# Performance work log

Measured on AMD Instinct MI355X. Metric: run time of the kernel, lower is better.

The kernel has to match this reference:

```python
import jax, jax.numpy as jnp
import numpy as np

B, D, NT, H, K = 4096, 112, 200, 512, 10
HID = 512
IN = 3 * D + NT + 1   # GRU input size = 537
M0 = H + 3 * D + NT   # MLP first-layer input = 1048


def setup_inputs() -> dict:
    key = jax.random.key(0)
    ks = jax.random.split(key, 9)
    def w(k, shape, fan):
        return jax.random.normal(k, shape, jnp.float32) / np.sqrt(fan).astype(np.float32)
    return {
        "z": jax.random.normal(ks[0], (B, D), jnp.float32),
        "c": jax.random.normal(ks[1], (B, D + NT), jnp.float32),
        "b": jax.random.uniform(ks[2], (B, D), jnp.float32),
        "m": jax.random.uniform(ks[3], (B, D), jnp.float32),
        "Wih": w(ks[4], (IN, 3 * H), IN),
        "Whh": w(ks[5], (H, 3 * H), H),
        "bih": jnp.zeros((3 * H,), jnp.float32),
        "bhh": jnp.zeros((3 * H,), jnp.float32),
        "W0": w(ks[6], (M0, HID), M0),
        "b0": jnp.zeros((HID,), jnp.float32),
        "W1": w(ks[7], (HID, HID), HID),
        "b1": jnp.zeros((HID,), jnp.float32),
        "W2": w(ks[8], (HID, 3 * K), HID),
        "b2": jnp.zeros((3 * K,), jnp.float32),
    }


def reference(z, c, b, m, Wih, Whh, bih, bhh, W0, b0, W1, b1, W2, b2):
    """AutoReg.logp: autoregressive GRU + MLP mixture-density head, gaussian base."""
    Bn = z.shape[0]
    const = jnp.concatenate([c, b, m], axis=1)          # [B, 3D+NT] fixed per step
    gi_const = const @ Wih[1:] + bih                    # input-proj of constant part
    w_z = Wih[0]                                        # [3H] weight for scalar z_t
    mlp_const = const @ W0[H:] + b0                     # const part of first MLP layer
    W0h = W0[:H]
    # teacher-forced previous-z sequence: z_0 = -1, then z[:, t-1]
    z_prev = jnp.concatenate([-jnp.ones((Bn, 1), z.dtype), z[:, :-1]], axis=1).T  # [D, B]

    def step(h, zt):  # h: [B,H], zt: [B]
        gi = zt[:, None] * w_z + gi_const               # [B, 3H]
        gh = h @ Whh + bhh
        ir, iz, inn = jnp.split(gi, 3, axis=1)
        hr, hz, hn = jnp.split(gh, 3, axis=1)
        r = jax.nn.sigmoid(ir + hr)
        u = jax.nn.sigmoid(iz + hz)
        n = jnp.tanh(inn + r * hn)
        h2 = (1.0 - u) * n + u * h                      # torch GRU update
        a = jnp.tanh(h2 @ W0h + mlp_const)              # Linear + Tanh on [h||c||b||m]
        a = jnp.tanh(a @ W1 + b1)
        p = a @ W2 + b2                                 # [B, 3K] mixture params
        return h2, p

    h0 = jnp.zeros((Bn, H), z.dtype)
    _, ps = jax.lax.scan(step, h0, z_prev)              # ps: [D, B, 3K]
    params = jnp.transpose(ps, (1, 0, 2))               # [B, D, 3K]

    logits, means, lsig = jnp.split(params, 3, axis=-1)
    sig = jnp.exp(lsig)
    t = z[..., None]
    log_norm = -lsig - 0.5 * np.float32(np.log(2.0 * np.pi))
    log_kern = -0.5 * jnp.square((t - means) / sig)
    ll = jax.nn.logsumexp(log_kern + log_norm + logits, axis=-1) \
         - jax.nn.logsumexp(logits, axis=-1)            # [B, D]

    query = m * (1.0 - b)
    mask = -jnp.sort(-query, axis=1)                    # descending sort values
    return jnp.sum(ll * mask, axis=1)                   # [B]
```

## Files before the change

kernel.cpp:

```cpp
#include <hip/hip_runtime.h>
#include <hip/hip_bf16.h>
#include <float.h>
#include <math.h>

#define BN   4096
#define DD   112
#define HH   512
#define G3   1536
#define CW   536
#define HIDD 512

typedef __attribute__((ext_vector_type(8))) short short8;
typedef __attribute__((ext_vector_type(4))) float float4v;

__device__ __forceinline__ unsigned short f2bf(float x) {
    __hip_bfloat16 h = __float2bfloat16(x);
    return *(unsigned short*)&h;
}

__global__ void build_const(const float* __restrict__ c, const float* __restrict__ b,
                            const float* __restrict__ m, float* __restrict__ out) {
    int idx = blockIdx.x * blockDim.x + threadIdx.x;
    if (idx >= BN * CW) return;
    int row = idx / CW, col = idx - row * CW;
    float v;
    if (col < 312)      v = c[row * 312 + col];
    else if (col < 424) v = b[row * 112 + (col - 312)];
    else                v = m[row * 112 + (col - 424)];
    out[idx] = v;
}

__global__ void zero_f32(float* __restrict__ p, int n) {
    int i = blockIdx.x * blockDim.x + threadIdx.x;
    if (i < n) p[i] = 0.0f;
}

__global__ __launch_bounds__(256) void gemm_bias(const float* __restrict__ A,
        const float* __restrict__ W, const float* __restrict__ bias,
        float* __restrict__ C, int N) {
    __shared__ float As[8][64];
    __shared__ float Ws[8][64];
    const int tid = threadIdx.x;
    const int tx = tid & 15, ty = tid >> 4;
    const int rowBase = blockIdx.x * 64, colBase = blockIdx.y * 64;
    float acc[4][4] = {};
    for (int kb = 0; kb < CW; kb += 8) {
        int l = tid * 2;
        {
            int i = l >> 3, j = l & 7;
            As[j][i] = A[(rowBase + i) * CW + kb + j];
            int i2 = (l + 1) >> 3, j2 = (l + 1) & 7;
            As[j2][i2] = A[(rowBase + i2) * CW + kb + j2];
        }
        {
            int j = l >> 6, n = l & 63;
            Ws[j][n] = W[(kb + j) * N + colBase + n];
            int j2 = (l + 1) >> 6, n2 = (l + 1) & 63;
            Ws[j2][n2] = W[(kb + j2) * N + colBase + n2];
        }
        __syncthreads();
#pragma unroll
        for (int k = 0; k < 8; ++k) {
            float av[4], wv[4];
#pragma unroll
            for (int i = 0; i < 4; ++i) av[i] = As[k][ty * 4 + i];
#pragma unroll
            for (int j = 0; j < 4; ++j) wv[j] = Ws[k][tx * 4 + j];
#pragma unroll
            for (int i = 0; i < 4; ++i)
#pragma unroll
                for (int j = 0; j < 4; ++j) acc[i][j] += av[i] * wv[j];
        }
        __syncthreads();
    }
#pragma unroll
    for (int i = 0; i < 4; ++i) {
        int r = rowBase + ty * 4 + i;
#pragma unroll
        for (int j = 0; j < 4; ++j) {
            int cc = colBase + tx * 4 + j;
            C[r * N + cc] = acc[i][j] + bias[cc];
        }
    }
}

__global__ void sort_mask(const float* __restrict__ b, const float* __restrict__ m,
                          float* __restrict__ maskbuf) {
    __shared__ float s[128];
    const int row = blockIdx.x, t = threadIdx.x;
    float v = -FLT_MAX;
    if (t < DD) v = m[row * DD + t] * (1.0f - b[row * DD + t]);
    s[t] = v;
    __syncthreads();
    for (int k = 2; k <= 128; k <<= 1) {
        for (int j = k >> 1; j > 0; j >>= 1) {
            int ixj = t ^ j;
            if (ixj > t) {
                bool up = ((t & k) == 0);
                float a = s[t], bb = s[ixj];
                if ((a > bb) == up) { s[t] = bb; s[ixj] = a; }
            }
            __syncthreads();
        }
    }
    if (t < DD) maskbuf[row * DD + t] = s[127 - t];
}

__global__ void pack_w(const float* __restrict__ src, unsigned short* __restrict__ dst,
                       int kchunks, int ldn, int ncols) {
    int bid = blockIdx.x;
    int nt = bid / kchunks, kc = bid - nt * kchunks;
    int lane = threadIdx.x;
    int quad = lane >> 4, l16 = lane & 15;
    int n = nt * 16 + l16;
    unsigned short v[8];
#pragma unroll
    for (int j = 0; j < 8; ++j) {
        int k = kc * 32 + quad * 8 + j;
        float f = (n < ncols) ? src[(size_t)k * ldn + n] : 0.0f;
        v[j] = f2bf(f);
    }
    unsigned short* p = dst + ((size_t)bid * 64 + lane) * 8;
#pragma unroll
    for (int j = 0; j < 8; ++j) p[j] = v[j];
}

__global__ __launch_bounds__(1024, 4) void gru_rec_chunk(
    const float* __restrict__ z, const float* __restrict__ Wih,
    const float* __restrict__ bhh, const float* __restrict__ gi_const,
    const unsigned short* __restrict__ WhhP,
    float* __restrict__ hstate, unsigned short* __restrict__ h2g,
    int t0, int tlen)
{
    __shared__ unsigned short h_bf[16 * 520];
    __shared__ float zbuf[113 * 16];

    const int tid = threadIdx.x;
    const int wave = tid >> 6, lane = tid & 63;
    const int quad = lane >> 4, l16 = lane & 15;
    const int rowBase = blockIdx.x * 16;

    for (int idx = tid; idx < 113 * 16; idx += 1024) {
        int tt = idx >> 4, r = idx & 15;
        zbuf[idx] = (tt == 0) ? -1.0f : z[(rowBase + r) * DD + tt - 1];
    }

    int hcol[2];
    float wz0[2], wz1[2], wz2[2], bh2r[2];
    float gic0[2][4], gic1[2][4], gic2[2][4];
    float h_own[2][4];
#pragma unroll
    for (int i = 0; i < 2; ++i) {
        int tile = wave + 16 * i;
        int hc = tile * 16 + l16;
        hcol[i] = hc;
        wz0[i] = Wih[hc]; wz1[i] = Wih[512 + hc]; wz2[i] = Wih[1024 + hc];
        float bh0 = bhh[hc], bh1 = bhh[512 + hc];
        bh2r[i] = bhh[1024 + hc];
#pragma unroll
        for (int rg = 0; rg < 4; ++rg) {
            int m = quad * 4 + rg;
            const float* g = gi_const + (size_t)(rowBase + m) * G3;
            gic0[i][rg] = g[hc] + bh0;
            gic1[i][rg] = g[512 + hc] + bh1;
            gic2[i][rg] = g[1024 + hc];
            float hv = hstate[(size_t)(rowBase + m) * HH + hc];
            h_own[i][rg] = hv;
            h_bf[m * 520 + hc] = f2bf(hv);
        }
    }
    const short8* WhhF = (const short8*)WhhP;
    __syncthreads();

    for (int tt = 0; tt < tlen; ++tt) {
        const int t = t0 + tt;
        float4v accR[2], accU[2], accN[2];
#pragma unroll
        for (int i = 0; i < 2; ++i) {
            accR[i] = (float4v){gic0[i][0], gic0[i][1], gic0[i][2], gic0[i][3]};
            accU[i] = (float4v){gic1[i][0], gic1[i][1], gic1[i][2], gic1[i][3]};
            accN[i] = (float4v){0.f, 0.f, 0.f, 0.f};
        }
#pragma unroll 4
        for (int kc = 0; kc < 16; ++kc) {
            short8 af = *(const short8*)&h_bf[l16 * 520 + kc * 32 + quad * 8];
#pragma unroll
            for (int i = 0; i < 2; ++i) {
                int tile = wave + 16 * i;
                accR[i] = __builtin_amdgcn_mfma_f32_16x16x32_bf16(af, WhhF[(tile * 16 + kc) * 64 + lane], accR[i], 0, 0, 0);
                accU[i] = __builtin_amdgcn_mfma_f32_16x16x32_bf16(af, WhhF[((tile + 32) * 16 + kc) * 64 + lane], accU[i], 0, 0, 0);
                accN[i] = __builtin_amdgcn_mfma_f32_16x16x32_bf16(af, WhhF[((tile + 64) * 16 + kc) * 64 + lane], accN[i], 0, 0, 0);
            }
        }
        __syncthreads();
#pragma unroll
        for (int i = 0; i < 2; ++i) {
#pragma unroll
            for (int rg = 0; rg < 4; ++rg) {
                int m = quad * 4 + rg;
                float zt = zbuf[t * 16 + m];
                float r = 1.0f / (1.0f + __expf(-(accR[i][rg] + zt * wz0[i])));
                float u = 1.0f / (1.0f + __expf(-(accU[i][rg] + zt * wz1[i])));
                float xn = gic2[i][rg] + zt * wz2[i] + r * (accN[i][rg] + bh2r[i]);
                float n = 1.0f - 2.0f / (__expf(2.0f * xn) + 1.0f);
                float h2 = (1.0f - u) * n + u * h_own[i][rg];
                h_own[i][rg] = h2;
                h_bf[m * 520 + hcol[i]] = f2bf(h2);
            }
        }
        __syncthreads();
        {
            int col = (lane) * 8;
            uint4 v = *(const uint4*)&h_bf[wave * 520 + col];
            *(uint4*)&h2g[((size_t)tt * BN + rowBase + wave) * 512 + col] = v;
        }
    }
#pragma unroll
    for (int i = 0; i < 2; ++i)
#pragma unroll
        for (int rg = 0; rg < 4; ++rg)
            hstate[(size_t)(rowBase + quad * 4 + rg) * HH + hcol[i]] = h_own[i][rg];
}

__global__ __launch_bounds__(1024, 4) void head_mdn(
    const float* __restrict__ z, const float* __restrict__ b1,
    const float* __restrict__ b2, const float* __restrict__ mlp_const,
    const float* __restrict__ maskbuf, const unsigned short* __restrict__ h2g,
    const unsigned short* __restrict__ W0hP, const unsigned short* __restrict__ W1P,
    const unsigned short* __restrict__ W2P, float* __restrict__ out, int t0)
{
    __shared__ unsigned short h_bf[32 * 520];
    __shared__ unsigned short a_bf[32 * 520];
    __shared__ float pp[16 * 512];

    const int tid = threadIdx.x;
    const int wave = tid >> 6, lane = tid & 63;
    const int quad = lane >> 4, l16 = lane & 15;
    const int pr = tid >> 5, pc = tid & 31;
    const int b0 = blockIdx.x * 2;
    const int tg = blockIdx.y;

    {
        int flat = tid * 16;
        int r = flat >> 9, col = flat & 511;
        int bb = b0 + (r >> 4), trel = tg * 16 + (r & 15);
        uint4 v0 = ((const uint4*)&h2g[((size_t)trel * BN + bb) * 512 + col])[0];
        uint4 v1 = ((const uint4*)&h2g[((size_t)trel * BN + bb) * 512 + col])[1];
        uint4* dst = (uint4*)&h_bf[r * 520 + col];
        dst[0] = v0; dst[1] = v1;
    }
    int hcol[2];
    float b1c[2], mlc[2][2];
#pragma unroll
    for (int i = 0; i < 2; ++i) {
        int hc = (wave + 16 * i) * 16 + l16;
        hcol[i] = hc;
        b1c[i] = b1[hc];
#pragma unroll
        for (int mt = 0; mt < 2; ++mt) mlc[i][mt] = mlp_const[(size_t)(b0 + mt) * HIDD + hc];
    }
    const float b2v = (pc < 30) ? b2[pc] : 0.0f;
    const int mdn_mt = pr >> 4, mdn_m = pr & 15;
    const int ppofs = (mdn_mt * 8) * 512 + (pc >> 4) * 256
                      + ((mdn_m >> 2) * 16 + (pc & 15)) * 4 + (mdn_m & 3);

    const short8* W0hF = (const short8*)W0hP;
    const short8* W1F  = (const short8*)W1P;
    const short8* W2F  = (const short8*)W2P;
    __syncthreads();

    float4v acc1[2][2];
#pragma unroll
    for (int i = 0; i < 2; ++i)
#pragma unroll
        for (int mt = 0; mt < 2; ++mt)
            acc1[i][mt] = (float4v){mlc[i][mt], mlc[i][mt], mlc[i][mt], mlc[i][mt]};
#pragma unroll 4
    for (int kc = 0; kc < 16; ++kc) {
        short8 af0 = *(const short8*)&h_bf[l16 * 520 + kc * 32 + quad * 8];
        short8 af1 = *(const short8*)&h_bf[(16 + l16) * 520 + kc * 32 + quad * 8];
#pragma unroll
        for (int i = 0; i < 2; ++i) {
            short8 bf = W0hF[((wave + 16 * i) * 16 + kc) * 64 + lane];
            acc1[i][0] = __builtin_amdgcn_mfma_f32_16x16x32_bf16(af0, bf, acc1[i][0], 0, 0, 0);
            acc1[i][1] = __builtin_amdgcn_mfma_f32_16x16x32_bf16(af1, bf, acc1[i][1], 0, 0, 0);
        }
    }
#pragma unroll
    for (int i = 0; i < 2; ++i)
#pragma unroll
        for (int mt = 0; mt < 2; ++mt)
#pragma unroll
            for (int rg = 0; rg < 4; ++rg) {
                int m = mt * 16 + quad * 4 + rg;
                float x = acc1[i][mt][rg];
                a_bf[m * 520 + hcol[i]] = f2bf(1.0f - 2.0f / (__expf(2.0f * x) + 1.0f));
            }
    __syncthreads();
    float4v acc2[2][2];
#pragma unroll
    for (int i = 0; i < 2; ++i)
#pragma unroll
        for (int mt = 0; mt < 2; ++mt)
            acc2[i][mt] = (float4v){b1c[i], b1c[i], b1c[i], b1c[i]};
#pragma unroll 4
    for (int kc = 0; kc < 16; ++kc) {
        short8 af0 = *(const short8*)&a_bf[l16 * 520 + kc * 32 + quad * 8];
        short8 af1 = *(const short8*)&a_bf[(16 + l16) * 520 + kc * 32 + quad * 8];
#pragma unroll
        for (int i = 0; i < 2; ++i) {
            short8 bf = W1F[((wave + 16 * i) * 16 + kc) * 64 + lane];
            acc2[i][0] = __builtin_amdgcn_mfma_f32_16x16x32_bf16(af0, bf, acc2[i][0], 0, 0, 0);
            acc2[i][1] = __builtin_amdgcn_mfma_f32_16x16x32_bf16(af1, bf, acc2[i][1], 0, 0, 0);
        }
    }
    __syncthreads();
#pragma unroll
    for (int i = 0; i < 2; ++i)
#pragma unroll
        for (int mt = 0; mt < 2; ++mt)
#pragma unroll
            for (int rg = 0; rg < 4; ++rg) {
                int m = mt * 16 + quad * 4 + rg;
                float x = acc2[i][mt][rg];
                a_bf[m * 520 + hcol[i]] = f2bf(1.0f - 2.0f / (__expf(2.0f * x) + 1.0f));
            }
    __syncthreads();
    {
        const int mtw = wave >> 3;
        float4v ap0 = (float4v){0.f, 0.f, 0.f, 0.f}, ap1 = (float4v){0.f, 0.f, 0.f, 0.f};
#pragma unroll
        for (int kk = 0; kk < 2; ++kk) {
            int kc = (wave & 7) * 2 + kk;
            short8 af = *(const short8*)&a_bf[(mtw * 16 + l16) * 520 + kc * 32 + quad * 8];
            ap0 = __builtin_amdgcn_mfma_f32_16x16x32_bf16(af, W2F[(0 * 16 + kc) * 64 + lane], ap0, 0, 0, 0);
            ap1 = __builtin_amdgcn_mfma_f32_16x16x32_bf16(af, W2F[(1 * 16 + kc) * 64 + lane], ap1, 0, 0, 0);
        }
#pragma unroll
        for (int rg = 0; rg < 4; ++rg) {
            pp[wave * 512 + 0 * 256 + lane * 4 + rg] = ap0[rg];
            pp[wave * 512 + 1 * 256 + lane * 4 + rg] = ap1[rg];
        }
    }
    __syncthreads();
    float llm;
    {
        float pv = b2v;
#pragma unroll
        for (int w = 0; w < 8; ++w) pv += pp[ppofs + w * 512];
        const int half = lane & 32;
        float meanv = __shfl(pv, half + ((pc + 10) & 31), 64);
        float lsigv = __shfl(pv, half + ((pc + 20) & 31), 64);
        float e1, e2;
        if (pc < 10) {
            float ztar = z[(size_t)(b0 + mdn_mt) * DD + t0 + tg * 16 + mdn_m];
            float invs = __expf(-lsigv);
            float dd = (ztar - meanv) * invs;
            e1 = -0.5f * dd * dd - lsigv - 0.91893853320467274f + pv;
            e2 = pv;
        } else { e1 = -FLT_MAX; e2 = -FLT_MAX; }
        float m1 = e1, m2 = e2;
#pragma unroll
        for (int off = 16; off > 0; off >>= 1) {
            m1 = fmaxf(m1, __shfl_xor(m1, off, 64));
            m2 = fmaxf(m2, __shfl_xor(m2, off, 64));
        }
        float s1 = (pc < 10) ? __expf(e1 - m1) : 0.0f;
        float s2 = (pc < 10) ? __expf(e2 - m2) : 0.0f;
#pragma unroll
        for (int off = 16; off > 0; off >>= 1) {
            s1 += __shfl_xor(s1, off, 64);
            s2 += __shfl_xor(s2, off, 64);
        }
        float ll = (m1 + __logf(s1)) - (m2 + __logf(s2));
        llm = ll * maskbuf[(size_t)(b0 + mdn_mt) * DD + t0 + tg * 16 + mdn_m];
    }
    __syncthreads();
    if (pc == 0) pp[pr] = llm;
    __syncthreads();
    if (tid < 2) {
        float s = 0.0f;
#pragma unroll
        for (int j = 0; j < 16; ++j) s += pp[tid * 16 + j];
        atomicAdd(&out[b0 + tid], s);
    }
}

__global__ __launch_bounds__(1024, 4) void gru_mfma_r5(
    const float* __restrict__ z, const float* __restrict__ Wih,
    const float* __restrict__ bhh, const float* __restrict__ b1,
    const float* __restrict__ b2,
    const float* __restrict__ gi_const, const float* __restrict__ mlp_const,
    const float* __restrict__ maskbuf,
    const unsigned short* __restrict__ WhhP, const unsigned short* __restrict__ W0hP,
    const unsigned short* __restrict__ W1P, const unsigned short* __restrict__ W2P,
    float* __restrict__ out)
{
    __shared__ unsigned short h_bf[16 * 520];
    __shared__ unsigned short a_bf[16 * 520];
    __shared__ float pp[16 * 512];
    __shared__ float zbuf[113 * 16];
    __shared__ float mbuf[16 * 112];

    const int tid = threadIdx.x;
    const int wave = tid >> 6, lane = tid & 63;
    const int quad = lane >> 4, l16 = lane & 15;
    const int pr = tid >> 5, pc = tid & 31;
    const int rowBase = blockIdx.x * 16;

    for (int idx = tid; idx < 16 * 520; idx += 1024) h_bf[idx] = 0;
    for (int idx = tid; idx < 113 * 16; idx += 1024) {
        int tt = idx >> 4, r = idx & 15;
        zbuf[idx] = (tt == 0) ? -1.0f : z[(rowBase + r) * DD + tt - 1];
    }
    for (int idx = tid; idx < 16 * 112; idx += 1024) {
        int r = idx / DD, tt = idx - r * DD;
        mbuf[idx] = maskbuf[(rowBase + r) * DD + tt];
    }
    int hcol[2];
    float wz0[2], wz1[2], wz2[2], bh2r[2], b1c[2];
    float gic0[2][4], gic1[2][4], gic2[2][4], mlc[2][4];
    float h_own[2][4];
#pragma unroll
    for (int i = 0; i < 2; ++i) {
        int tile = wave + 16 * i;
        int hc = tile * 16 + l16;
        hcol[i] = hc;
        wz0[i] = Wih[hc]; wz1[i] = Wih[512 + hc]; wz2[i] = Wih[1024 + hc];
        float bh0 = bhh[hc], bh1 = bhh[512 + hc];
        bh2r[i] = bhh[1024 + hc];
        b1c[i] = b1[hc];
#pragma unroll
        for (int rg = 0; rg < 4; ++rg) {
            int m = quad * 4 + rg;
            const float* g = gi_const + (size_t)(rowBase + m) * G3;
            gic0[i][rg] = g[hc] + bh0;
            gic1[i][rg] = g[512 + hc] + bh1;
            gic2[i][rg] = g[1024 + hc];
            mlc[i][rg] = mlp_const[(size_t)(rowBase + m) * HIDD + hc];
            h_own[i][rg] = 0.0f;
        }
    }
    const float b2v = (pc < 30) ? b2[pc] : 0.0f;
    const int ppbase = (pc >> 4) * 256 + ((pr >> 2) * 16 + (pc & 15)) * 4 + (pr & 3);
    const short8* WhhF = (const short8*)WhhP;
    const short8* W0hF = (const short8*)W0hP;
    const short8* W1F  = (const short8*)W1P;
    const short8* W2F  = (const short8*)W2P;
    float llacc = 0.0f;
    __syncthreads();
    for (int t = 0; t < DD; ++t) {
        float4v accR[2], accU[2], accN[2];
#pragma unroll
        for (int i = 0; i < 2; ++i) {
            accR[i] = (float4v){gic0[i][0], gic0[i][1], gic0[i][2], gic0[i][3]};
            accU[i] = (float4v){gic1[i][0], gic1[i][1], gic1[i][2], gic1[i][3]};
            accN[i] = (float4v){0.f, 0.f, 0.f, 0.f};
        }
#pragma unroll 4
        for (int kc = 0; kc < 16; ++kc) {
            short8 af = *(const short8*)&h_bf[l16 * 520 + kc * 32 + quad * 8];
#pragma unroll
            for (int i = 0; i < 2; ++i) {
                int tile = wave + 16 * i;
                accR[i] = __builtin_amdgcn_mfma_f32_16x16x32_bf16(af, WhhF[(tile * 16 + kc) * 64 + lane], accR[i], 0, 0, 0);
                accU[i] = __builtin_amdgcn_mfma_f32_16x16x32_bf16(af, WhhF[((tile + 32) * 16 + kc) * 64 + lane], accU[i], 0, 0, 0);
                accN[i] = __builtin_amdgcn_mfma_f32_16x16x32_bf16(af, WhhF[((tile + 64) * 16 + kc) * 64 + lane], accN[i], 0, 0, 0);
            }
        }
        __syncthreads();
#pragma unroll
        for (int i = 0; i < 2; ++i) {
#pragma unroll
            for (int rg = 0; rg < 4; ++rg) {
                int m = quad * 4 + rg;
                float zt = zbuf[t * 16 + m];
                float r = 1.0f / (1.0f + __expf(-(accR[i][rg] + zt * wz0[i])));
                float u = 1.0f / (1.0f + __expf(-(accU[i][rg] + zt * wz1[i])));
                float xn = gic2[i][rg] + zt * wz2[i] + r * (accN[i][rg] + bh2r[i]);
                float n = 1.0f - 2.0f / (__expf(2.0f * xn) + 1.0f);
                float h2 = (1.0f - u) * n + u * h_own[i][rg];
                h_own[i][rg] = h2;
                h_bf[m * 520 + hcol[i]] = f2bf(h2);
            }
        }
        __syncthreads();
        float4v acc1[2];
#pragma unroll
        for (int i = 0; i < 2; ++i) acc1[i] = (float4v){mlc[i][0], mlc[i][1], mlc[i][2], mlc[i][3]};
#pragma unroll 4
        for (int kc = 0; kc < 16; ++kc) {
            short8 af = *(const short8*)&h_bf[l16 * 520 + kc * 32 + quad * 8];
#pragma unroll
            for (int i = 0; i < 2; ++i)
                acc1[i] = __builtin_amdgcn_mfma_f32_16x16x32_bf16(af, W0hF[((wave + 16 * i) * 16 + kc) * 64 + lane], acc1[i], 0, 0, 0);
        }
#pragma unroll
        for (int i = 0; i < 2; ++i)
#pragma unroll
            for (int rg = 0; rg < 4; ++rg) {
                int m = quad * 4 + rg;
                float x = acc1[i][rg];
                a_bf[m * 520 + hcol[i]] = f2bf(1.0f - 2.0f / (__expf(2.0f * x) + 1.0f));
            }
        __syncthreads();
        float4v acc2[2];
#pragma unroll
        for (int i = 0; i < 2; ++i) acc2[i] = (float4v){b1c[i], b1c[i], b1c[i], b1c[i]};
#pragma unroll 4
        for (int kc = 0; kc < 16; ++kc) {
            short8 af = *(const short8*)&a_bf[l16 * 520 + kc * 32 + quad * 8];
#pragma unroll
            for (int i = 0; i < 2; ++i)
                acc2[i] = __builtin_amdgcn_mfma_f32_16x16x32_bf16(af, W1F[((wave + 16 * i) * 16 + kc) * 64 + lane], acc2[i], 0, 0, 0);
        }
        __syncthreads();
#pragma unroll
        for (int i = 0; i < 2; ++i)
#pragma unroll
            for (int rg = 0; rg < 4; ++rg) {
                int m = quad * 4 + rg;
                float x = acc2[i][rg];
                a_bf[m * 520 + hcol[i]] = f2bf(1.0f - 2.0f / (__expf(2.0f * x) + 1.0f));
            }
        __syncthreads();
        {
            int kc = wave;
            short8 af = *(const short8*)&a_bf[l16 * 520 + kc * 32 + quad * 8];
            float4v ap0 = (float4v){0.f, 0.f, 0.f, 0.f}, ap1 = (float4v){0.f, 0.f, 0.f, 0.f};
            ap0 = __builtin_amdgcn_mfma_f32_16x16x32_bf16(af, W2F[(0 * 16 + kc) * 64 + lane], ap0, 0, 0, 0);
            ap1 = __builtin_amdgcn_mfma_f32_16x16x32_bf16(af, W2F[(1 * 16 + kc) * 64 + lane], ap1, 0, 0, 0);
#pragma unroll
            for (int rg = 0; rg < 4; ++rg) {
                pp[wave * 512 + 0 * 256 + lane * 4 + rg] = ap0[rg];
                pp[wave * 512 + 1 * 256 + lane * 4 + rg] = ap1[rg];
            }
        }
        __syncthreads();
        if (wave < 8) {
            float pv = b2v;
#pragma unroll
            for (int w = 0; w < 16; ++w) pv += pp[w * 512 + ppbase];
            const int half = lane & 32;
            float meanv = __shfl(pv, half + ((pc + 10) & 31), 64);
            float lsigv = __shfl(pv, half + ((pc + 20) & 31), 64);
            float e1, e2;
            if (pc < 10) {
                float ztar = zbuf[(t + 1) * 16 + pr];
                float invs = __expf(-lsigv);
                float dd = (ztar - meanv) * invs;
                e1 = -0.5f * dd * dd - lsigv - 0.91893853320467274f + pv;
                e2 = pv;
            } else { e1 = -FLT_MAX; e2 = -FLT_MAX; }
            float m1 = e1, m2 = e2;
#pragma unroll
            for (int off = 16; off > 0; off >>= 1) {
                m1 = fmaxf(m1, __shfl_xor(m1, off, 64));
                m2 = fmaxf(m2, __shfl_xor(m2, off, 64));
            }
            float s1 = (pc < 10) ? __expf(e1 - m1) : 0.0f;
            float s2 = (pc < 10) ? __expf(e2 - m2) : 0.0f;
#pragma unroll
            for (int off = 16; off > 0; off >>= 1) {
                s1 += __shfl_xor(s1, off, 64);
                s2 += __shfl_xor(s2, off, 64);
            }
            float ll = (m1 + __logf(s1)) - (m2 + __logf(s2));
            llacc += ll * mbuf[pr * 112 + t];
        }
    }
    if (wave < 8 && pc == 0) out[rowBase + pr] = llacc;
}

extern "C" void kernel_launch(void* const* d_in, const int* in_sizes, int n_in,
                              void* d_out, int out_size, void* d_ws, size_t ws_size,
                              hipStream_t stream) {
    const float* z   = (const float*)d_in[0];
    const float* c   = (const float*)d_in[1];
    const float* b   = (const float*)d_in[2];
    const float* m   = (const float*)d_in[3];
    const float* Wih = (const float*)d_in[4];
    const float* Whh = (const float*)d_in[5];
    const float* bih = (const float*)d_in[6];
    const float* bhh = (const float*)d_in[7];
    const float* W0  = (const float*)d_in[8];
    const float* b0  = (const float*)d_in[9];
    const float* W1  = (const float*)d_in[10];
    const float* b1  = (const float*)d_in[11];
    const float* W2  = (const float*)d_in[12];
    const float* b2  = (const float*)d_in[13];
    float* out = (float*)d_out;

    float* ws        = (float*)d_ws;
    float* constbuf  = ws;
    float* gi_const  = constbuf + (size_t)BN * CW;
    float* mlp_const = gi_const + (size_t)BN * G3;
    float* maskbuf   = mlp_const + (size_t)BN * HIDD;
    unsigned short* WhhP = (unsigned short*)(maskbuf + (size_t)BN * DD);
    unsigned short* W0hP = WhhP + (size_t)96 * 16 * 512;
    unsigned short* W1P  = W0hP + (size_t)32 * 16 * 512;
    unsigned short* W2P  = W1P  + (size_t)32 * 16 * 512;
    float* hstate        = (float*)(W2P + (size_t)2 * 16 * 512);
    unsigned short* h2g  = (unsigned short*)(hstate + (size_t)BN * HH);

    const size_t base = (size_t)BN * (CW + G3 + HIDD + DD) * 4
                      + (size_t)(96 + 32 + 32 + 2) * 16 * 512 * 2
                      + (size_t)BN * HH * 4;
    const size_t slab_per_t = (size_t)BN * 512 * 2;
    int TC = 0;
    if (ws_size > base) {
        TC = (int)((ws_size - base) / slab_per_t);
        TC = (TC / 16) * 16;
        if (TC > DD) TC = DD;
    }

    build_const<<<(BN * CW + 255) / 256, 256, 0, stream>>>(c, b, m, constbuf);
    dim3 g1(BN / 64, G3 / 64);
    gemm_bias<<<g1, 256, 0, stream>>>(constbuf, Wih + G3, bih, gi_const, G3);
    dim3 g2(BN / 64, HIDD / 64);
    gemm_bias<<<g2, 256, 0, stream>>>(constbuf, W0 + (size_t)HH * HIDD, b0, mlp_const, HIDD);
    sort_mask<<<BN, 128, 0, stream>>>(b, m, maskbuf);
    pack_w<<<96 * 16, 64, 0, stream>>>(Whh, WhhP, 16, G3, G3);
    pack_w<<<32 * 16, 64, 0, stream>>>(W0,  W0hP, 16, HIDD, HIDD);
    pack_w<<<32 * 16, 64, 0, stream>>>(W1,  W1P,  16, HIDD, HIDD);
    pack_w<<<2 * 16, 64, 0, stream>>>(W2,  W2P,  16, 30, 30);

    if (TC >= 16) {
        zero_f32<<<(BN * HH + 255) / 256, 256, 0, stream>>>(hstate, BN * HH);
        zero_f32<<<(BN + 255) / 256, 256, 0, stream>>>(out, BN);
        for (int t0 = 0; t0 < DD; t0 += TC) {
            int tlen = DD - t0 < TC ? DD - t0 : TC;
            gru_rec_chunk<<<BN / 16, 1024, 0, stream>>>(z, Wih, bhh, gi_const, WhhP,
                                                        hstate, h2g, t0, tlen);
            dim3 gh(BN / 2, tlen / 16);
            head_mdn<<<gh, 1024, 0, stream>>>(z, b1, b2, mlp_const, maskbuf, h2g,
                                              W0hP, W1P, W2P, out, t0);
        }
    } else {
        gru_mfma_r5<<<BN / 16, 1024, 0, stream>>>(z, Wih, bhh, b1, b2, gi_const,
                                                  mlp_const, maskbuf, WhhP, W0hP, W1P, W2P, out);
    }
}
```

Before: 2.971 ms.

## Use MFMA for constant projections, double-buffer GRU hidden state, widen head tile

Replaces the scalar fp32 tiled GEMMs for the constant input projections with bf16 MFMA kernels over a padded bf16 const buffer and pre-packed weights. The GRU recurrence double-buffers the bf16 hidden state in LDS to drop one barrier per step and unrolls the k loop further. The MDN head now processes 64 rows per block (4 batch rows x 16 steps), reusing weight fragments across more M tiles and reusing LDS for partials. The constant projections lose some precision by moving to bf16, and the larger head tile raises register and LDS pressure.

```diff
diff --git a/kernel.cpp b/kernel.cpp
--- a/kernel.cpp
+++ b/kernel.cpp
@@ -8,6 +8,7 @@
 #define HH   512
 #define G3   1536
 #define CW   536
+#define CWP  544
 #define HIDD 512
 
 typedef __attribute__((ext_vector_type(8))) short short8;
@@ -18,16 +19,17 @@
     return *(unsigned short*)&h;
 }
 
-__global__ void build_const(const float* __restrict__ c, const float* __restrict__ b,
-                            const float* __restrict__ m, float* __restrict__ out) {
+__global__ void build_constbf(const float* __restrict__ c, const float* __restrict__ b,
+                              const float* __restrict__ m, unsigned short* __restrict__ out) {
     int idx = blockIdx.x * blockDim.x + threadIdx.x;
-    if (idx >= BN * CW) return;
-    int row = idx / CW, col = idx - row * CW;
+    if (idx >= BN * CWP) return;
+    int row = idx / CWP, col = idx - row * CWP;
     float v;
     if (col < 312)      v = c[row * 312 + col];
     else if (col < 424) v = b[row * 112 + (col - 312)];
-    else                v = m[row * 112 + (col - 424)];
-    out[idx] = v;
+    else if (col < 536) v = m[row * 112 + (col - 424)];
+    else                v = 0.0f;
+    out[idx] = f2bf(v);
 }
 
 __global__ void zero_f32(float* __restrict__ p, int n) {
@@ -35,52 +37,56 @@
     if (i < n) p[i] = 0.0f;
 }
 
-__global__ __launch_bounds__(256) void gemm_bias(const float* __restrict__ A,
-        const float* __restrict__ W, const float* __restrict__ bias,
-        float* __restrict__ C, int N) {
-    __shared__ float As[8][64];
-    __shared__ float Ws[8][64];
+__global__ void pack_wN(const float* __restrict__ src, unsigned short* __restrict__ dst,
+                        int kchunks, int ldn, int ncols, int nrows) {
+    int bid = blockIdx.x;
+    int nt = bid / kchunks, kc = bid - nt * kchunks;
+    int lane = threadIdx.x;
+    int quad = lane >> 4, l16 = lane & 15;
+    int n = nt * 16 + l16;
+    unsigned short v[8];
+#pragma unroll
+    for (int j = 0; j < 8; ++j) {
+        int k = kc * 32 + quad * 8 + j;
+        float f = (k < nrows && n < ncols) ? src[(size_t)k * ldn + n] : 0.0f;
+        v[j] = f2bf(f);
+    }
+    unsigned short* p = dst + ((size_t)bid * 64 + lane) * 8;
+#pragma unroll
+    for (int j = 0; j < 8; ++j) p[j] = v[j];
+}
+
+template<int TPW>
+__global__ __launch_bounds__(1024) void gemm_const_mfma(
+    const unsigned short* __restrict__ A, const unsigned short* __restrict__ BP,
+    const float* __restrict__ bias, float* __restrict__ C, int N)
+{
     const int tid = threadIdx.x;
-    const int tx = tid & 15, ty = tid >> 4;
-    const int rowBase = blockIdx.x * 64, colBase = blockIdx.y * 64;
-    float acc[4][4] = {};
-    for (int kb = 0; kb < CW; kb += 8) {
-        int l = tid * 2;
-        {
-            int i = l >> 3, j = l & 7;
-            As[j][i] = A[(rowBase + i) * CW + kb + j];
-            int i2 = (l + 1) >> 3, j2 = (l + 1) & 7;
-            As[j2][i2] = A[(rowBase + i2) * CW + kb + j2];
-        }
-        {
-            int j = l >> 6, n = l & 63;
-            Ws[j][n] = W[(kb + j) * N + colBase + n];
-            int j2 = (l + 1) >> 6, n2 = (l + 1) & 63;
-            Ws[j2][n2] = W[(kb + j2) * N + colBase + n2];
-        }
-        __syncthreads();
-#pragma unroll
-        for (int k = 0; k < 8; ++k) {
-            float av[4], wv[4];
-#pragma unroll
-            for (int i = 0; i < 4; ++i) av[i] = As[k][ty * 4 + i];
-#pragma unroll
-            for (int j = 0; j < 4; ++j) wv[j] = Ws[k][tx * 4 + j];
-#pragma unroll
-            for (int i = 0; i < 4; ++i)
-#pragma unroll
-                for (int j = 0; j < 4; ++j) acc[i][j] += av[i] * wv[j];
-        }
-        __syncthreads();
-    }
-#pragma unroll
-    for (int i = 0; i < 4; ++i) {
-        int r = rowBase + ty * 4 + i;
-#pragma unroll
-        for (int j = 0; j < 4; ++j) {
-            int cc = colBase + tx * 4 + j;
-            C[r * N + cc] = acc[i][j] + bias[cc];
-        }
+    const int wave = tid >> 6, lane = tid & 63;
+    const int quad = lane >> 4, l16 = lane & 15;
+    const int rowBase = blockIdx.x * 16;
+    const short8* BF = (const short8*)BP;
+    float4v acc[TPW];
+#pragma unroll
+    for (int i = 0; i < TPW; ++i) {
+        float bv = bias[(wave + 16 * i) * 16 + l16];
+        acc[i] = (float4v){bv, bv, bv, bv};
+    }
+#pragma unroll 4
+    for (int kc = 0; kc < 17; ++kc) {
+        short8 af = *(const short8*)&A[(size_t)(rowBase + l16) * CWP + kc * 32 + quad * 8];
+#pragma unroll
+        for (int i = 0; i < TPW; ++i) {
+            int tile = wave + 16 * i;
+            acc[i] = __builtin_amdgcn_mfma_f32_16x16x32_bf16(af, BF[(tile * 17 + kc) * 64 + lane], acc[i], 0, 0, 0);
+        }
+    }
+#pragma unroll
+    for (int i = 0; i < TPW; ++i) {
+        int col = (wave + 16 * i) * 16 + l16;
+#pragma unroll
+        for (int rg = 0; rg < 4; ++rg)
+            C[(size_t)(rowBase + quad * 4 + rg) * N + col] = acc[i][rg];
     }
 }
 
@@ -106,25 +112,6 @@
     if (t < DD) maskbuf[row * DD + t] = s[127 - t];
 }
 
-__global__ void pack_w(const float* __restrict__ src, unsigned short* __restrict__ dst,
-                       int kchunks, int ldn, int ncols) {
-    int bid = blockIdx.x;
-    int nt = bid / kchunks, kc = bid - nt * kchunks;
-    int lane = threadIdx.x;
-    int quad = lane >> 4, l16 = lane & 15;
-    int n = nt * 16 + l16;
-    unsigned short v[8];
-#pragma unroll
-    for (int j = 0; j < 8; ++j) {
-        int k = kc * 32 + quad * 8 + j;
-        float f = (n < ncols) ? src[(size_t)k * ldn + n] : 0.0f;
-        v[j] = f2bf(f);
-    }
-    unsigned short* p = dst + ((size_t)bid * 64 + lane) * 8;
-#pragma unroll
-    for (int j = 0; j < 8; ++j) p[j] = v[j];
-}
-
 __global__ __launch_bounds__(1024, 4) void gru_rec_chunk(
     const float* __restrict__ z, const float* __restrict__ Wih,
     const float* __restrict__ bhh, const float* __restrict__ gi_const,
@@ -132,7 +119,7 @@
     float* __restrict__ hstate, unsigned short* __restrict__ h2g,
     int t0, int tlen)
 {
-    __shared__ unsigned short h_bf[16 * 520];
+    __shared__ unsigned short h_bf[2][16 * 520];
     __shared__ float zbuf[113 * 16];
 
     const int tid = threadIdx.x;
@@ -166,7 +153,7 @@
             gic2[i][rg] = g[1024 + hc];
             float hv = hstate[(size_t)(rowBase + m) * HH + hc];
             h_own[i][rg] = hv;
-            h_bf[m * 520 + hc] = f2bf(hv);
+            h_bf[0][m * 520 + hc] = f2bf(hv);
         }
     }
     const short8* WhhF = (const short8*)WhhP;
@@ -174,6 +161,9 @@
 
     for (int tt = 0; tt < tlen; ++tt) {
         const int t = t0 + tt;
+        const int p = tt & 1;
+        const unsigned short* hsrc = h_bf[p];
+        unsigned short* hdst = h_bf[p ^ 1];
         float4v accR[2], accU[2], accN[2];
 #pragma unroll
         for (int i = 0; i < 2; ++i) {
@@ -181,9 +171,9 @@
             accU[i] = (float4v){gic1[i][0], gic1[i][1], gic1[i][2], gic1[i][3]};
             accN[i] = (float4v){0.f, 0.f, 0.f, 0.f};
         }
-#pragma unroll 4
+#pragma unroll 8
         for (int kc = 0; kc < 16; ++kc) {
-            short8 af = *(const short8*)&h_bf[l16 * 520 + kc * 32 + quad * 8];
+            short8 af = *(const short8*)&hsrc[l16 * 520 + kc * 32 + quad * 8];
 #pragma unroll
             for (int i = 0; i < 2; ++i) {
                 int tile = wave + 16 * i;
@@ -192,7 +182,6 @@
                 accN[i] = __builtin_amdgcn_mfma_f32_16x16x32_bf16(af, WhhF[((tile + 64) * 16 + kc) * 64 + lane], accN[i], 0, 0, 0);
             }
         }
-        __syncthreads();
 #pragma unroll
         for (int i = 0; i < 2; ++i) {
 #pragma unroll
@@ -205,13 +194,13 @@
                 float n = 1.0f - 2.0f / (__expf(2.0f * xn) + 1.0f);
                 float h2 = (1.0f - u) * n + u * h_own[i][rg];
                 h_own[i][rg] = h2;
-                h_bf[m * 520 + hcol[i]] = f2bf(h2);
+                hdst[m * 520 + hcol[i]] = f2bf(h2);
             }
         }
         __syncthreads();
         {
-            int col = (lane) * 8;
-            uint4 v = *(const uint4*)&h_bf[wave * 520 + col];
+            int col = lane * 8;
+            uint4 v = *(const uint4*)&hdst[wave * 520 + col];
             *(uint4*)&h2g[((size_t)tt * BN + rowBase + wave) * 512 + col] = v;
         }
     }
@@ -222,74 +211,73 @@
             hstate[(size_t)(rowBase + quad * 4 + rg) * HH + hcol[i]] = h_own[i][rg];
 }
 
-__global__ __launch_bounds__(1024, 4) void head_mdn(
+__global__ __launch_bounds__(1024) void head_mdn64(
     const float* __restrict__ z, const float* __restrict__ b1,
     const float* __restrict__ b2, const float* __restrict__ mlp_const,
     const float* __restrict__ maskbuf, const unsigned short* __restrict__ h2g,
     const unsigned short* __restrict__ W0hP, const unsigned short* __restrict__ W1P,
     const unsigned short* __restrict__ W2P, float* __restrict__ out, int t0)
 {
-    __shared__ unsigned short h_bf[32 * 520];
-    __shared__ unsigned short a_bf[32 * 520];
-    __shared__ float pp[16 * 512];
+    __shared__ unsigned short h_bf[64 * 520];
+    __shared__ unsigned short a_bf[64 * 520];
+    float* ppf = (float*)a_bf;
 
     const int tid = threadIdx.x;
     const int wave = tid >> 6, lane = tid & 63;
     const int quad = lane >> 4, l16 = lane & 15;
     const int pr = tid >> 5, pc = tid & 31;
-    const int b0 = blockIdx.x * 2;
+    const int b0 = blockIdx.x * 4;
     const int tg = blockIdx.y;
 
     {
-        int flat = tid * 16;
+        int flat = tid * 32;
         int r = flat >> 9, col = flat & 511;
         int bb = b0 + (r >> 4), trel = tg * 16 + (r & 15);
-        uint4 v0 = ((const uint4*)&h2g[((size_t)trel * BN + bb) * 512 + col])[0];
-        uint4 v1 = ((const uint4*)&h2g[((size_t)trel * BN + bb) * 512 + col])[1];
+        const uint4* src = (const uint4*)&h2g[((size_t)trel * BN + bb) * 512 + col];
+        uint4 v0 = src[0], v1 = src[1], v2 = src[2], v3 = src[3];
         uint4* dst = (uint4*)&h_bf[r * 520 + col];
-        dst[0] = v0; dst[1] = v1;
+        dst[0] = v0; dst[1] = v1; dst[2] = v2; dst[3] = v3;
     }
     int hcol[2];
-    float b1c[2], mlc[2][2];
+    float b1c[2], mlc[2][4];
 #pragma unroll
     for (int i = 0; i < 2; ++i) {
         int hc = (wave + 16 * i) * 16 + l16;
         hcol[i] = hc;
         b1c[i] = b1[hc];
 #pragma unroll
-        for (int mt = 0; mt < 2; ++mt) mlc[i][mt] = mlp_const[(size_t)(b0 + mt) * HIDD + hc];
+        for (int mt = 0; mt < 4; ++mt) mlc[i][mt] = mlp_const[(size_t)(b0 + mt) * HIDD + hc];
     }
     const float b2v = (pc < 30) ? b2[pc] : 0.0f;
-    const int mdn_mt = pr >> 4, mdn_m = pr & 15;
-    const int ppofs = (mdn_mt * 8) * 512 + (pc >> 4) * 256
-                      + ((mdn_m >> 2) * 16 + (pc & 15)) * 4 + (mdn_m & 3);
-
     const short8* W0hF = (const short8*)W0hP;
     const short8* W1F  = (const short8*)W1P;
     const short8* W2F  = (const short8*)W2P;
     __syncthreads();
 
-    float4v acc1[2][2];
+    float4v acc1[2][4];
 #pragma unroll
     for (int i = 0; i < 2; ++i)
 #pragma unroll
-        for (int mt = 0; mt < 2; ++mt)
+        for (int mt = 0; mt < 4; ++mt)
             acc1[i][mt] = (float4v){mlc[i][mt], mlc[i][mt], mlc[i][mt], mlc[i][mt]};
-#pragma unroll 4
+#pragma unroll 2
     for (int kc = 0; kc < 16; ++kc) {
-        short8 af0 = *(const short8*)&h_bf[l16 * 520 + kc * 32 + quad * 8];
-        short8 af1 = *(const short8*)&h_bf[(16 + l16) * 520 + kc * 32 + quad * 8];
+        short8 af[4];
+#pragma unroll
+        for (int mt = 0; mt < 4; ++mt)
+            af[mt] = *(const short8*)&h_bf[(mt * 16 + l16) * 520 + kc * 32 + quad * 8];
 #pragma unroll
         for (int i = 0; i < 2; ++i) {
             short8 bf = W0hF[((wave + 16 * i) * 16 + kc) * 64 + lane];
-            acc1[i][0] = __builtin_amdgcn_mfma_f32_16x16x32_bf16(af0, bf, acc1[i][0], 0, 0, 0);
-            acc1[i][1] = __builtin_amdgcn_mfma_f32_16x16x32_bf16(af1, bf, acc1[i][1], 0, 0, 0);
+#pragma unroll
+            for (int mt = 0; mt < 4; ++mt)
+                acc1[i][mt] = __builtin_amdgcn_mfma_f32_16x16x32_bf16(af[mt], bf, acc1[i][mt], 0, 0, 0);
         }
     }
 #pragma unroll
     for (int i = 0; i < 2; ++i)
 #pragma unroll
-        for (int mt = 0; mt < 2; ++mt)
+        for (int mt = 0; mt < 4; ++mt)
 #pragma unroll
             for (int rg = 0; rg < 4; ++rg) {
                 int m = mt * 16 + quad * 4 + rg;
@@ -297,63 +285,73 @@
                 a_bf[m * 520 + hcol[i]] = f2bf(1.0f - 2.0f / (__expf(2.0f * x) + 1.0f));
             }
     __syncthreads();
-    float4v acc2[2][2];
+    float4v acc2[2][4];
 #pragma unroll
     for (int i = 0; i < 2; ++i)
 #pragma unroll
-        for (int mt = 0; mt < 2; ++mt)
+        for (int mt = 0; mt < 4; ++mt)
             acc2[i][mt] = (float4v){b1c[i], b1c[i], b1c[i], b1c[i]};
-#pragma unroll 4
+#pragma unroll 2
     for (int kc = 0; kc < 16; ++kc) {
-        short8 af0 = *(const short8*)&a_bf[l16 * 520 + kc * 32 + quad * 8];
-        short8 af1 = *(const short8*)&a_bf[(16 + l16) * 520 + kc * 32 + quad * 8];
+        short8 af[4];
+#pragma unroll
+        for (int mt = 0; mt < 4; ++mt)
+            af[mt] = *(const short8*)&a_bf[(mt * 16 + l16) * 520 + kc * 32 + quad * 8];
 #pragma unroll
         for (int i = 0; i < 2; ++i) {
             short8 bf = W1F[((wave + 16 * i) * 16 + kc) * 64 + lane];
-            acc2[i][0] = __builtin_amdgcn_mfma_f32_16x16x32_bf16(af0, bf, acc2[i][0], 0, 0, 0);
-            acc2[i][1] = __builtin_amdgcn_mfma_f32_16x16x32_bf16(af1, bf, acc2[i][1], 0, 0, 0);
+#pragma unroll
+            for (int mt = 0; mt < 4; ++mt)
+                acc2[i][mt] = __builtin_amdgcn_mfma_f32_16x16x32_bf16(af[mt], bf, acc2[i][mt], 0, 0, 0);
         }
     }
     __syncthreads();
 #pragma unroll
     for (int i = 0; i < 2; ++i)
 #pragma unroll
-        for (int mt = 0; mt < 2; ++mt)
+        for (int mt = 0; mt < 4; ++mt)
 #pragma unroll
             for (int rg = 0; rg < 4; ++rg) {
                 int m = mt * 16 + quad * 4 + rg;
                 float x = acc2[i][mt][rg];
-                a_bf[m * 520 + hcol[i]] = f2bf(1.0f - 2.0f / (__expf(2.0f * x) + 1.0f));
+                h_bf[m * 520 + hcol[i]] = f2bf(1.0f - 2.0f / (__expf(2.0f * x) + 1.0f));
             }
     __syncthreads();
     {
-        const int mtw = wave >> 3;
+        const int mtw = wave >> 2, kg = wave & 3;
         float4v ap0 = (float4v){0.f, 0.f, 0.f, 0.f}, ap1 = (float4v){0.f, 0.f, 0.f, 0.f};
 #pragma unroll
-        for (int kk = 0; kk < 2; ++kk) {
-            int kc = (wave & 7) * 2 + kk;
-            short8 af = *(const short8*)&a_bf[(mtw * 16 + l16) * 520 + kc * 32 + quad * 8];
+        for (int kk = 0; kk < 4; ++kk) {
+            int kc = kg * 4 + kk;
+            short8 af = *(const short8*)&h_bf[(mtw * 16 + l16) * 520 + kc * 32 + quad * 8];
             ap0 = __builtin_amdgcn_mfma_f32_16x16x32_bf16(af, W2F[(0 * 16 + kc) * 64 + lane], ap0, 0, 0, 0);
             ap1 = __builtin_amdgcn_mfma_f32_16x16x32_bf16(af, W2F[(1 * 16 + kc) * 64 + lane], ap1, 0, 0, 0);
         }
 #pragma unroll
         for (int rg = 0; rg < 4; ++rg) {
-            pp[wave * 512 + 0 * 256 + lane * 4 + rg] = ap0[rg];
-            pp[wave * 512 + 1 * 256 + lane * 4 + rg] = ap1[rg];
-        }
-    }
-    __syncthreads();
-    float llm;
-    {
+            ppf[((kg * 4 + mtw) * 2 + 0) * 256 + lane * 4 + rg] = ap0[rg];
+            ppf[((kg * 4 + mtw) * 2 + 1) * 256 + lane * 4 + rg] = ap1[rg];
+        }
+    }
+    __syncthreads();
+    float llm[2];
+#pragma unroll
+    for (int rh = 0; rh < 2; ++rh) {
+        const int slot = rh * 32 + pr;
+        const int bsub = slot >> 4, toff = slot & 15;
+        const int mm = slot & 15;
+        const int lane_c = ((mm >> 2) * 16 + (pc & 15));
+        const int rgc = mm & 3, ntv = pc >> 4;
         float pv = b2v;
 #pragma unroll
-        for (int w = 0; w < 8; ++w) pv += pp[ppofs + w * 512];
+        for (int kg = 0; kg < 4; ++kg)
+            pv += ppf[((kg * 4 + bsub) * 2 + ntv) * 256 + lane_c * 4 + rgc];
         const int half = lane & 32;
         float meanv = __shfl(pv, half + ((pc + 10) & 31), 64);
         float lsigv = __shfl(pv, half + ((pc + 20) & 31), 64);
         float e1, e2;
         if (pc < 10) {
-            float ztar = z[(size_t)(b0 + mdn_mt) * DD + t0 + tg * 16 + mdn_m];
+            float ztar = z[(size_t)(b0 + bsub) * DD + t0 + tg * 16 + toff];
             float invs = __expf(-lsigv);
             float dd = (ztar - meanv) * invs;
             e1 = -0.5f * dd * dd - lsigv - 0.91893853320467274f + pv;
@@ -373,15 +371,15 @@
             s2 += __shfl_xor(s2, off, 64);
         }
         float ll = (m1 + __logf(s1)) - (m2 + __logf(s2));
-        llm = ll * maskbuf[(size_t)(b0 + mdn_mt) * DD + t0 + tg * 16 + mdn_m];
-    }
-    __syncthreads();
-    if (pc == 0) pp[pr] = llm;
-    __syncthreads();
-    if (tid < 2) {
+        llm[rh] = ll * maskbuf[(size_t)(b0 + bsub) * DD + t0 + tg * 16 + toff];
+    }
+    __syncthreads();
+    if (pc == 0) { ppf[pr] = llm[0]; ppf[32 + pr] = llm[1]; }
+    __syncthreads();
+    if (tid < 4) {
         float s = 0.0f;
 #pragma unroll
-        for (int j = 0; j < 16; ++j) s += pp[tid * 16 + j];
+        for (int j = 0; j < 16; ++j) s += ppf[tid * 16 + j];
         atomicAdd(&out[b0 + tid], s);
     }
 }
@@ -591,21 +589,21 @@
     const float* b2  = (const float*)d_in[13];
     float* out = (float*)d_out;
 
-    float* ws        = (float*)d_ws;
-    float* constbuf  = ws;
-    float* gi_const  = constbuf + (size_t)BN * CW;
-    float* mlp_const = gi_const + (size_t)BN * G3;
-    float* maskbuf   = mlp_const + (size_t)BN * HIDD;
-    unsigned short* WhhP = (unsigned short*)(maskbuf + (size_t)BN * DD);
-    unsigned short* W0hP = WhhP + (size_t)96 * 16 * 512;
-    unsigned short* W1P  = W0hP + (size_t)32 * 16 * 512;
-    unsigned short* W2P  = W1P  + (size_t)32 * 16 * 512;
-    float* hstate        = (float*)(W2P + (size_t)2 * 16 * 512);
-    unsigned short* h2g  = (unsigned short*)(hstate + (size_t)BN * HH);
-
-    const size_t base = (size_t)BN * (CW + G3 + HIDD + DD) * 4
-                      + (size_t)(96 + 32 + 32 + 2) * 16 * 512 * 2
-                      + (size_t)BN * HH * 4;
+    char* p = (char*)d_ws;
+    unsigned short* constbf = (unsigned short*)p;  p += (size_t)BN * CWP * 2;
+    float* gi_const  = (float*)p;                  p += (size_t)BN * G3 * 4;
+    float* mlp_const = (float*)p;                  p += (size_t)BN * HIDD * 4;
+    float* maskbuf   = (float*)p;                  p += (size_t)BN * DD * 4;
+    unsigned short* WihP = (unsigned short*)p;     p += (size_t)96 * 17 * 512 * 2;
+    unsigned short* W0cP = (unsigned short*)p;     p += (size_t)32 * 17 * 512 * 2;
+    unsigned short* WhhP = (unsigned short*)p;     p += (size_t)96 * 16 * 512 * 2;
+    unsigned short* W0hP = (unsigned short*)p;     p += (size_t)32 * 16 * 512 * 2;
+    unsigned short* W1P  = (unsigned short*)p;     p += (size_t)32 * 16 * 512 * 2;
+    unsigned short* W2P  = (unsigned short*)p;     p += (size_t)2 * 16 * 512 * 2;
+    float* hstate        = (float*)p;              p += (size_t)BN * HH * 4;
+    unsigned short* h2g  = (unsigned short*)p;
+
+    const size_t base = (size_t)(p - (char*)d_ws);
     const size_t slab_per_t = (size_t)BN * 512 * 2;
     int TC = 0;
     if (ws_size > base) {
@@ -614,16 +612,16 @@
         if (TC > DD) TC = DD;
     }
 
-    build_const<<<(BN * CW + 255) / 256, 256, 0, stream>>>(c, b, m, constbuf);
-    dim3 g1(BN / 64, G3 / 64);
-    gemm_bias<<<g1, 256, 0, stream>>>(constbuf, Wih + G3, bih, gi_const, G3);
-    dim3 g2(BN / 64, HIDD / 64);
-    gemm_bias<<<g2, 256, 0, stream>>>(constbuf, W0 + (size_t)HH * HIDD, b0, mlp_const, HIDD);
+    build_constbf<<<(BN * CWP + 255) / 256, 256, 0, stream>>>(c, b, m, constbf);
+    pack_wN<<<96 * 17, 64, 0, stream>>>(Wih + G3, WihP, 17, G3, G3, CW);
+    pack_wN<<<32 * 17, 64, 0, stream>>>(W0 + (size_t)HH * HIDD, W0cP, 17, HIDD, HIDD, CW);
+    pack_wN<<<96 * 16, 64, 0, stream>>>(Whh, WhhP, 16, G3, G3, HH);
+    pack_wN<<<32 * 16, 64, 0, stream>>>(W0,  W0hP, 16, HIDD, HIDD, HH);
+    pack_wN<<<32 * 16, 64, 0, stream>>>(W1,  W1P,  16, HIDD, HIDD, HH);
+    pack_wN<<<2 * 16, 64, 0, stream>>>(W2,  W2P,  16, 30, 30, HH);
+    gemm_const_mfma<6><<<BN / 16, 1024, 0, stream>>>(constbf, WihP, bih, gi_const, G3);
+    gemm_const_mfma<2><<<BN / 16, 1024, 0, stream>>>(constbf, W0cP, b0, mlp_const, HIDD);
     sort_mask<<<BN, 128, 0, stream>>>(b, m, maskbuf);
-    pack_w<<<96 * 16, 64, 0, stream>>>(Whh, WhhP, 16, G3, G3);
-    pack_w<<<32 * 16, 64, 0, stream>>>(W0,  W0hP, 16, HIDD, HIDD);
-    pack_w<<<32 * 16, 64, 0, stream>>>(W1,  W1P,  16, HIDD, HIDD);
-    pack_w<<<2 * 16, 64, 0, stream>>>(W2,  W2P,  16, 30, 30);
 
     if (TC >= 16) {
         zero_f32<<<(BN * HH + 255) / 256, 256, 0, stream>>>(hstate, BN * HH);
@@ -632,9 +630,9 @@
             int tlen = DD - t0 < TC ? DD - t0 : TC;
             gru_rec_chunk<<<BN / 16, 1024, 0, stream>>>(z, Wih, bhh, gi_const, WhhP,
                                                         hstate, h2g, t0, tlen);
-            dim3 gh(BN / 2, tlen / 16);
-            head_mdn<<<gh, 1024, 0, stream>>>(z, b1, b2, mlp_const, maskbuf, h2g,
-                                              W0hP, W1P, W2P, out, t0);
+            dim3 gh(BN / 4, tlen / 16);
+            head_mdn64<<<gh, 1024, 0, stream>>>(z, b1, b2, mlp_const, maskbuf, h2g,
+                                                W0hP, W1P, W2P, out, t0);
         }
     } else {
         gru_mfma_r5<<<BN / 16, 1024, 0, stream>>>(z, Wih, bhh, b1, b2, gi_const,
```

Measured after the change: 2.642 ms. 11.1% less time.
